# Kernel optimization log

Measured on AMD Instinct MI355X. Metric: run time of the kernel, lower is better.

Reference implementation:

```python
import jax, jax.numpy as jnp
import numpy as np

FORGET_BIAS = 1.0  # TF BasicLSTMCell default

B, T, D, H = 64, 1024, 300, 512


def setup_inputs() -> dict:
    key = jax.random.key(0)
    k1, k2, k3 = jax.random.split(key, 3)
    essays = jax.random.normal(k1, (B, T, D), dtype=jnp.float32)
    # TF BasicLSTMCell: single kernel [D+H, 4H], gate order (i, j, f, o)
    W_lstm = jax.random.normal(k2, (D + H, 4 * H), dtype=jnp.float32) * 0.05
    b_lstm = jnp.zeros((4 * H,), dtype=jnp.float32)
    W_dense = jax.random.normal(k3, (H, 1), dtype=jnp.float32) * 0.05
    b_dense = jnp.zeros((1,), dtype=jnp.float32)
    return {"essays": essays, "W_lstm": W_lstm, "b_lstm": b_lstm,
            "W_dense": W_dense, "b_dense": b_dense}


def _lstm_scan(essays, W_lstm, b_lstm):
    # Precompute input projection for all timesteps: [B,T,4H]
    Wx, Wh = W_lstm[:D], W_lstm[D:]
    x_proj = jnp.einsum('btd,dg->btg', essays, Wx) + b_lstm

    def step(carry, xp):
        c, h = carry
        gates = xp + h @ Wh  # [B,4H]
        i, j, f, o = jnp.split(gates, 4, axis=-1)
        new_c = c * jax.nn.sigmoid(f + FORGET_BIAS) + jax.nn.sigmoid(i) * jnp.tanh(j)
        new_h = jnp.tanh(new_c) * jax.nn.sigmoid(o)
        return (new_c, new_h), new_h

    init = (jnp.zeros((essays.shape[0], H), essays.dtype),
            jnp.zeros((essays.shape[0], H), essays.dtype))
    _, hs = jax.lax.scan(step, init, jnp.swapaxes(x_proj, 0, 1))  # hs: [T,B,H]
    return jnp.swapaxes(hs, 0, 1)  # [B,T,H]


def reference(essays, W_lstm, b_lstm, W_dense, b_dense):
    lstm_out = _lstm_scan(essays, W_lstm, b_lstm)      # [B,T,H]
    mot = jnp.mean(lstm_out, axis=1)                   # mean-over-time pooling [B,H]
    preds = jax.nn.sigmoid(mot @ W_dense + b_dense)    # [B,1]
    return preds.reshape(-1)                           # [B]
```

## Files before the change

kernel.cpp:

```cpp
#include <hip/hip_runtime.h>
#include <hip/hip_bf16.h>
#include <stdint.h>

#define B_   64
#define T_   1024
#define D_   300
#define H_   512
#define G4H  2048
#define KP   320

typedef __attribute__((ext_vector_type(8))) short short8;
typedef __attribute__((ext_vector_type(4))) float f32x4;
typedef unsigned long long ull;

__device__ __forceinline__ unsigned short f2bf(float v) {
    __hip_bfloat16 h = __float2bfloat16(v);
    return *reinterpret_cast<unsigned short*>(&h);
}
__device__ __forceinline__ float bf2f(unsigned u) {
    return __uint_as_float(u << 16);
}
__device__ __forceinline__ float sigm(float x) { return 1.f / (1.f + __expf(-x)); }
__device__ __forceinline__ float tanhfast(float x) {
    float e = __expf(2.f * x);
    return 1.f - 2.f / (e + 1.f);
}

#define ASYNC16(g, l)                                                        \
    __builtin_amdgcn_global_load_lds(                                        \
        (const __attribute__((address_space(1))) void*)(g),                  \
        (__attribute__((address_space(3))) void*)(l), 16, 0, 0)

__global__ void cvt_essays(const float* __restrict__ es, unsigned short* __restrict__ Ab) {
    unsigned i = blockIdx.x * 256u + threadIdx.x;
    unsigned row = i / KP;
    unsigned col = i - row * KP;
    float v = (col < D_) ? es[(size_t)row * D_ + col] : 0.f;
    Ab[i] = f2bf(v);
}

__global__ void cvt_misc(const float* __restrict__ Wl, unsigned short* __restrict__ Bt) {
    unsigned i = blockIdx.x * 256u + threadIdx.x;
    unsigned n = i / KP, k = i - n * KP;
    float v = (k < D_) ? Wl[(size_t)k * G4H + n] : 0.f;
    Bt[i] = f2bf(v);
}

__global__ void cvt_wh(const float* __restrict__ Wl, unsigned short* __restrict__ WhTg) {
    unsigned i = blockIdx.x * 256u + threadIdx.x;
    unsigned gc = i & 2047u, k = i >> 11;
    WhTg[(size_t)gc * 512 + k] = f2bf(Wl[(size_t)(300 + k) * G4H + gc]);
}

__global__ __launch_bounds__(256) void gemm_xp(
    const unsigned short* __restrict__ Ab,
    const unsigned short* __restrict__ Bt,
    const float* __restrict__ bias,
    unsigned short* __restrict__ xpr)
{
    __shared__ __align__(16) unsigned short Al[128 * 32];
    __shared__ __align__(16) unsigned short Bl[128 * 32];
    const int tid = threadIdx.x;
    const int w = tid >> 6, lane = tid & 63;
    const int ln = lane & 15, q = lane >> 4;
    const int bx = blockIdx.x;
    const int m0 = (bx >> 4) * 128;
    const int n0 = (bx & 15) * 128;
    const int wr = w >> 1, wc = w & 1;

    f32x4 acc[4][4];
#pragma unroll
    for (int i = 0; i < 4; i++)
#pragma unroll
        for (int j = 0; j < 4; j++) acc[i][j] = (f32x4){0.f, 0.f, 0.f, 0.f};

    for (int k0 = 0; k0 < KP; k0 += 32) {
#pragma unroll
        for (int it = 0; it < 2; ++it) {
            int s = it * 4 + w;
            int c = s * 64 + lane;
            int r = c >> 2;
            int ko = (c & 3) * 8;
            ASYNC16(Ab + (size_t)(m0 + r) * KP + k0 + ko, &Al[s * 512]);
            ASYNC16(Bt + (size_t)(n0 + r) * KP + k0 + ko, &Bl[s * 512]);
        }
        __syncthreads();
        short8 af[4], bf[4];
#pragma unroll
        for (int mt = 0; mt < 4; ++mt)
            af[mt] = *(const short8*)&Al[(wr * 64 + mt * 16 + ln) * 32 + q * 8];
#pragma unroll
        for (int nt = 0; nt < 4; ++nt)
            bf[nt] = *(const short8*)&Bl[(wc * 64 + nt * 16 + ln) * 32 + q * 8];
#pragma unroll
        for (int mt = 0; mt < 4; ++mt)
#pragma unroll
            for (int nt = 0; nt < 4; ++nt)
                acc[mt][nt] = __builtin_amdgcn_mfma_f32_16x16x32_bf16(af[mt], bf[nt], acc[mt][nt], 0, 0, 0);
        __syncthreads();
    }
#pragma unroll
    for (int mt = 0; mt < 4; ++mt) {
#pragma unroll
        for (int nt = 0; nt < 4; ++nt) {
            int col = n0 + wc * 64 + nt * 16 + ln;
            int gate = col >> 9, r9 = col & 511;
            int slice = r9 >> 4, jj = r9 & 15;
            float bb = bias[col];
#pragma unroll
            for (int r = 0; r < 4; ++r) {
                int row = m0 + wr * 64 + mt * 16 + q * 4 + r;
                int t = row & 1023, bglob = row >> 10;
                int g = bglob >> 4, bloc = bglob & 15;
                size_t idx = ((((size_t)t * 4 + g) * 32 + slice) * 16 + bloc) * 64
                             + gate * 16 + jj;
                xpr[idx] = f2bf(acc[mt][nt][r] + bb);
            }
        }
    }
}

__global__ __launch_bounds__(256, 1) void lstm_rec(
    const unsigned short* __restrict__ WhTg,
    const unsigned short* __restrict__ xpr,
    unsigned* __restrict__ hfp,
    float* __restrict__ hmean)
{
    __shared__ __align__(16) unsigned short WhT[64 * 520];
    __shared__ __align__(16) unsigned short hl[16 * 520];
    __shared__ float gbuf[4][16][17];

    const int tid = threadIdx.x;
    const int bid = blockIdx.x;
    const int g     = bid >> 5;
    const int slice = bid & 31;
    const int j0    = slice * 16;
    const int bg    = g * 16;
    const int wv = tid >> 6, lane = tid & 63, ln = lane & 15, q = lane >> 4;

    for (int ch = tid; ch < 64 * 64; ch += 256) {
        int c = ch >> 6, off = (ch & 63) * 8;
        int gc = (c >> 4) * 512 + j0 + (c & 15);
        *(uint4*)&WhT[c * 520 + off] = *(const uint4*)&WhTg[(size_t)gc * 512 + off];
    }

    const int b = tid >> 4;
    const int j = tid & 15;
    const int rowoff = (bg + b) * 512;

    {
        ull* hl8 = (ull*)hl;
#pragma unroll
        for (int i = 0; i < 16; ++i) {
            int c = tid + (i << 8);
            int row = c >> 8, pair = c & 255;
            hl8[(row * 1040 + pair * 8) >> 3] = 0ull;
        }
    }

    float c_st = 0.f, hsum = 0.f;
    const unsigned short* xblk0 = xpr + ((size_t)g * 32 + slice) * 1024 + b * 64 + j;
    unsigned short xc0 = xblk0[0], xc1 = xblk0[16], xc2 = xblk0[32], xc3 = xblk0[48];
    unsigned short xn0 = xc0, xn1 = xc1, xn2 = xc2, xn3 = xc3;

    for (int t = 0; t < T_; ++t) {
        if (t + 1 < T_) {
            const unsigned short* xr = xblk0 + (size_t)(t + 1) * 131072;
            xn0 = xr[0]; xn1 = xr[16]; xn2 = xr[32]; xn3 = xr[48];
        }
        if (t > 0) {
            const ull* src = (const ull*)(hfp + (size_t)(t & 1) * 32768 + bg * 512);
            const unsigned want = (unsigned)((t >> 1) & 3);
            ull v[16];
#pragma unroll
            for (int i = 0; i < 16; ++i)
                v[i] = __hip_atomic_load(src + tid + (i << 8),
                                         __ATOMIC_RELAXED, __HIP_MEMORY_SCOPE_AGENT);
            while (true) {
                unsigned bad = 0u;
#pragma unroll
                for (int i = 0; i < 16; ++i) {
                    unsigned lo = (unsigned)v[i], hi = (unsigned)(v[i] >> 32);
                    bad |= ((((lo & 3u) ^ want) | ((hi & 3u) ^ want)) != 0u) ? (1u << i) : 0u;
                }
                if (!bad) break;
#pragma unroll
                for (int i = 0; i < 16; ++i)
                    if (bad & (1u << i))
                        v[i] = __hip_atomic_load(src + tid + (i << 8),
                                                 __ATOMIC_RELAXED, __HIP_MEMORY_SCOPE_AGENT);
            }
#pragma unroll
            for (int i = 0; i < 16; ++i) {
                int c = tid + (i << 8);
                int row = c >> 8, pair = c & 255;
                unsigned u = (unsigned)f2bf(__uint_as_float((unsigned)v[i]))
                           | ((unsigned)f2bf(__uint_as_float((unsigned)(v[i] >> 32))) << 16);
                *(unsigned*)((char*)hl + row * 1040 + pair * 4) = u;
            }
        }
        __syncthreads();

        f32x4 acc = (f32x4){0.f, 0.f, 0.f, 0.f};
#pragma unroll
        for (int kk = 0; kk < 16; ++kk) {
            short8 av = *(const short8*)&hl[ln * 520 + kk * 32 + q * 8];
            short8 bv = *(const short8*)&WhT[(wv * 16 + ln) * 520 + kk * 32 + q * 8];
            acc = __builtin_amdgcn_mfma_f32_16x16x32_bf16(av, bv, acc, 0, 0, 0);
        }
#pragma unroll
        for (int r = 0; r < 4; ++r)
            gbuf[wv][q * 4 + r][ln] = acc[r];
        __syncthreads();

        float ai  = gbuf[0][b][j] + bf2f((unsigned)xc0);
        float aj  = gbuf[1][b][j] + bf2f((unsigned)xc1);
        float af_ = gbuf[2][b][j] + bf2f((unsigned)xc2);
        float ao  = gbuf[3][b][j] + bf2f((unsigned)xc3);
        float si = sigm(ai), tj = tanhfast(aj);
        float sf = sigm(af_ + 1.0f), so = sigm(ao);
        c_st = c_st * sf + si * tj;
        float h = tanhfast(c_st) * so;
        hsum += h;
        xc0 = xn0; xc1 = xn1; xc2 = xn2; xc3 = xn3;

        unsigned hb = (__float_as_uint(h) & ~3u) | (unsigned)(((t + 1) >> 1) & 3);
        __hip_atomic_store(hfp + (size_t)((t + 1) & 1) * 32768 + rowoff + j0 + j,
                           hb, __ATOMIC_RELAXED, __HIP_MEMORY_SCOPE_AGENT);
    }
    hmean[(size_t)rowoff + j0 + j] = hsum * (1.f / 1024.f);
}

__global__ void dense_out(const float* __restrict__ hmean, const float* __restrict__ Wd,
                          const float* __restrict__ bd, float* __restrict__ out) {
    int bb = blockIdx.x;
    int lane = threadIdx.x;
    float p = 0.f;
    for (int e = lane; e < H_; e += 64) p += hmean[(size_t)bb * H_ + e] * Wd[e];
#pragma unroll
    for (int off = 32; off; off >>= 1) p += __shfl_down(p, off);
    if (lane == 0) out[bb] = 1.f / (1.f + __expf(-(p + bd[0])));
}

extern "C" void kernel_launch(void* const* d_in, const int* in_sizes, int n_in,
                              void* d_out, int out_size, void* d_ws, size_t ws_size,
                              hipStream_t stream) {
    const float* essays  = (const float*)d_in[0];
    const float* W_lstm  = (const float*)d_in[1];
    const float* b_lstm  = (const float*)d_in[2];
    const float* W_dense = (const float*)d_in[3];
    const float* b_dense = (const float*)d_in[4];
    float* out = (float*)d_out;

    char* ws = (char*)d_ws;
    unsigned short* xp   = (unsigned short*)(ws);
    unsigned short* Ab   = (unsigned short*)(ws + 268435456ull);
    unsigned short* Bt   = (unsigned short*)(ws + 310378496ull);
    unsigned short* WhTg = (unsigned short*)(ws + 311689216ull);
    unsigned*       hfp  = (unsigned*)(ws + 268435456ull);
    float*          hm   = (float*)(ws + 268435456ull + 262144ull);

    hipLaunchKernelGGL(cvt_essays, dim3(81920), dim3(256), 0, stream, essays, Ab);
    hipLaunchKernelGGL(cvt_misc,   dim3(2560),  dim3(256), 0, stream, W_lstm, Bt);
    hipLaunchKernelGGL(cvt_wh,     dim3(4096),  dim3(256), 0, stream, W_lstm, WhTg);
    hipLaunchKernelGGL(gemm_xp,    dim3(8192),  dim3(256), 0, stream, Ab, Bt, b_lstm, xp);
    hipLaunchKernelGGL(lstm_rec,   dim3(128),   dim3(256), 0, stream, WhTg, xp, hfp, hm);
    hipLaunchKernelGGL(dense_out,  dim3(64),    dim3(64),  0, stream, hm, W_dense, b_dense, out);
}
```

Before: 3.620 ms.

## Restructure LSTM recurrence into single-wave blocks with register weights and swizzled bf16 h exchange

The recurrent kernel moves from 256-thread blocks to one 64-lane wave per block. The Wh slice now lives in registers instead of LDS, and all four gate accumulators are computed by the same wave, which removes both __syncthreads and the gate-staging buffer. Hidden state is exchanged as bf16 with a 16-bit timestep tag in a layout pre-swizzled to match the MFMA A-operand. Each chunk is polled and fed straight into the MFMA, so waiting overlaps with compute. The xproj layout is interleaved per gate for 64-bit loads. The trade-offs are heavy register pressure (64 short8 weights plus 64 ull loads) and a 16-bit tag that wraps only beyond 65535 steps.

```diff
diff --git a/kernel.cpp b/kernel.cpp
--- a/kernel.cpp
+++ b/kernel.cpp
@@ -31,6 +31,8 @@
         (const __attribute__((address_space(1))) void*)(g),                  \
         (__attribute__((address_space(3))) void*)(l), 16, 0, 0)
 
+#define ALD(p) __hip_atomic_load((p), __ATOMIC_RELAXED, __HIP_MEMORY_SCOPE_AGENT)
+
 __global__ void cvt_essays(const float* __restrict__ es, unsigned short* __restrict__ Ab) {
     unsigned i = blockIdx.x * 256u + threadIdx.x;
     unsigned row = i / KP;
@@ -46,10 +48,12 @@
     Bt[i] = f2bf(v);
 }
 
-__global__ void cvt_wh(const float* __restrict__ Wl, unsigned short* __restrict__ WhTg) {
+__global__ void cvt_wh(const float* __restrict__ Wl, unsigned short* __restrict__ WhTg,
+                       unsigned* __restrict__ hswz) {
     unsigned i = blockIdx.x * 256u + threadIdx.x;
     unsigned gc = i & 2047u, k = i >> 11;
     WhTg[(size_t)gc * 512 + k] = f2bf(Wl[(size_t)(300 + k) * G4H + gc]);
+    if (i < 65536u) hswz[i] = 0x0000FFFFu;
 }
 
 __global__ __launch_bounds__(256) void gemm_xp(
@@ -113,122 +117,122 @@
                 int t = row & 1023, bglob = row >> 10;
                 int g = bglob >> 4, bloc = bglob & 15;
                 size_t idx = ((((size_t)t * 4 + g) * 32 + slice) * 16 + bloc) * 64
-                             + gate * 16 + jj;
+                             + jj * 4 + gate;
                 xpr[idx] = f2bf(acc[mt][nt][r] + bb);
             }
         }
     }
 }
 
-__global__ __launch_bounds__(256, 1) void lstm_rec(
+__global__ __launch_bounds__(64, 1) void lstm_rec(
     const unsigned short* __restrict__ WhTg,
     const unsigned short* __restrict__ xpr,
-    unsigned* __restrict__ hfp,
+    unsigned* __restrict__ hswz,
     float* __restrict__ hmean)
 {
-    __shared__ __align__(16) unsigned short WhT[64 * 520];
-    __shared__ __align__(16) unsigned short hl[16 * 520];
-    __shared__ float gbuf[4][16][17];
-
-    const int tid = threadIdx.x;
     const int bid = blockIdx.x;
     const int g     = bid >> 5;
     const int slice = bid & 31;
     const int j0    = slice * 16;
     const int bg    = g * 16;
-    const int wv = tid >> 6, lane = tid & 63, ln = lane & 15, q = lane >> 4;
-
-    for (int ch = tid; ch < 64 * 64; ch += 256) {
-        int c = ch >> 6, off = (ch & 63) * 8;
-        int gc = (c >> 4) * 512 + j0 + (c & 15);
-        *(uint4*)&WhT[c * 520 + off] = *(const uint4*)&WhTg[(size_t)gc * 512 + off];
-    }
-
-    const int b = tid >> 4;
-    const int j = tid & 15;
-    const int rowoff = (bg + b) * 512;
-
-    {
-        ull* hl8 = (ull*)hl;
-#pragma unroll
-        for (int i = 0; i < 16; ++i) {
-            int c = tid + (i << 8);
-            int row = c >> 8, pair = c & 255;
-            hl8[(row * 1040 + pair * 8) >> 3] = 0ull;
-        }
-    }
-
-    float c_st = 0.f, hsum = 0.f;
-    const unsigned short* xblk0 = xpr + ((size_t)g * 32 + slice) * 1024 + b * 64 + j;
-    unsigned short xc0 = xblk0[0], xc1 = xblk0[16], xc2 = xblk0[32], xc3 = xblk0[48];
-    unsigned short xn0 = xc0, xn1 = xc1, xn2 = xc2, xn3 = xc3;
+    const int lane = threadIdx.x, ln = lane & 15, q = lane >> 4;
+
+    short8 bw[64];
+#pragma unroll
+    for (int gate = 0; gate < 4; ++gate)
+#pragma unroll
+        for (int kk = 0; kk < 16; ++kk)
+            bw[gate * 16 + kk] =
+                *(const short8*)&WhTg[(size_t)(gate * 512 + j0 + ln) * 512 + kk * 32 + q * 8];
+
+    float c_[4] = {0.f, 0.f, 0.f, 0.f};
+    float hs[4] = {0.f, 0.f, 0.f, 0.f};
+
+    const int csrc = g * 4096 + q * 64 + ln * 4;
+    const int kel = j0 + ln;
+    const int sdst = g * 8192 + (kel >> 5) * 512 + ((kel >> 3) & 3) * 128 + q * 32 + (kel & 7);
+
+    const unsigned short* xreg0 = xpr + ((size_t)g * 32 + slice) * 1024;
+    ull xc[4], xn[4];
+#pragma unroll
+    for (int r = 0; r < 4; ++r)
+        xc[r] = *(const ull*)(xreg0 + (4 * q + r) * 64 + ln * 4);
 
     for (int t = 0; t < T_; ++t) {
         if (t + 1 < T_) {
-            const unsigned short* xr = xblk0 + (size_t)(t + 1) * 131072;
-            xn0 = xr[0]; xn1 = xr[16]; xn2 = xr[32]; xn3 = xr[48];
-        }
+            const unsigned short* xr = xreg0 + (size_t)(t + 1) * 131072;
+#pragma unroll
+            for (int r = 0; r < 4; ++r)
+                xn[r] = *(const ull*)(xr + (4 * q + r) * 64 + ln * 4);
+        }
+
+        f32x4 acc0 = (f32x4){0.f, 0.f, 0.f, 0.f};
+        f32x4 acc1 = (f32x4){0.f, 0.f, 0.f, 0.f};
+        f32x4 acc2 = (f32x4){0.f, 0.f, 0.f, 0.f};
+        f32x4 acc3 = (f32x4){0.f, 0.f, 0.f, 0.f};
+
         if (t > 0) {
-            const ull* src = (const ull*)(hfp + (size_t)(t & 1) * 32768 + bg * 512);
-            const unsigned want = (unsigned)((t >> 1) & 3);
-            ull v[16];
-#pragma unroll
-            for (int i = 0; i < 16; ++i)
-                v[i] = __hip_atomic_load(src + tid + (i << 8),
-                                         __ATOMIC_RELAXED, __HIP_MEMORY_SCOPE_AGENT);
-            while (true) {
-                unsigned bad = 0u;
-#pragma unroll
-                for (int i = 0; i < 16; ++i) {
-                    unsigned lo = (unsigned)v[i], hi = (unsigned)(v[i] >> 32);
-                    bad |= ((((lo & 3u) ^ want) | ((hi & 3u) ^ want)) != 0u) ? (1u << i) : 0u;
+            const ull* hb = (const ull*)hswz + (size_t)(t & 1) * 16384 + csrc;
+            const unsigned wt = (unsigned)t;
+            ull v[64];
+#pragma unroll
+            for (int kk = 0; kk < 16; ++kk)
+#pragma unroll
+                for (int i = 0; i < 4; ++i)
+                    v[kk * 4 + i] = ALD(hb + kk * 256 + i);
+#pragma unroll
+            for (int kk = 0; kk < 16; ++kk) {
+                ull a0 = v[kk * 4], a1 = v[kk * 4 + 1], a2 = v[kk * 4 + 2], a3 = v[kk * 4 + 3];
+                unsigned bad =
+                    (((unsigned)a0 ^ wt) | ((unsigned)(a0 >> 32) ^ wt) |
+                     ((unsigned)a1 ^ wt) | ((unsigned)(a1 >> 32) ^ wt) |
+                     ((unsigned)a2 ^ wt) | ((unsigned)(a2 >> 32) ^ wt) |
+                     ((unsigned)a3 ^ wt) | ((unsigned)(a3 >> 32) ^ wt)) & 0xffffu;
+                while (bad != 0u) {
+                    a0 = ALD(hb + kk * 256);
+                    a1 = ALD(hb + kk * 256 + 1);
+                    a2 = ALD(hb + kk * 256 + 2);
+                    a3 = ALD(hb + kk * 256 + 3);
+                    bad =
+                        (((unsigned)a0 ^ wt) | ((unsigned)(a0 >> 32) ^ wt) |
+                         ((unsigned)a1 ^ wt) | ((unsigned)(a1 >> 32) ^ wt) |
+                         ((unsigned)a2 ^ wt) | ((unsigned)(a2 >> 32) ^ wt) |
+                         ((unsigned)a3 ^ wt) | ((unsigned)(a3 >> 32) ^ wt)) & 0xffffu;
                 }
-                if (!bad) break;
-#pragma unroll
-                for (int i = 0; i < 16; ++i)
-                    if (bad & (1u << i))
-                        v[i] = __hip_atomic_load(src + tid + (i << 8),
-                                                 __ATOMIC_RELAXED, __HIP_MEMORY_SCOPE_AGENT);
+                union { unsigned u[4]; short8 s; } cv;
+                cv.u[0] = __builtin_amdgcn_perm((unsigned)(a0 >> 32), (unsigned)a0, 0x07060302u);
+                cv.u[1] = __builtin_amdgcn_perm((unsigned)(a1 >> 32), (unsigned)a1, 0x07060302u);
+                cv.u[2] = __builtin_amdgcn_perm((unsigned)(a2 >> 32), (unsigned)a2, 0x07060302u);
+                cv.u[3] = __builtin_amdgcn_perm((unsigned)(a3 >> 32), (unsigned)a3, 0x07060302u);
+                short8 af = cv.s;
+                acc0 = __builtin_amdgcn_mfma_f32_16x16x32_bf16(af, bw[kk],      acc0, 0, 0, 0);
+                acc1 = __builtin_amdgcn_mfma_f32_16x16x32_bf16(af, bw[16 + kk], acc1, 0, 0, 0);
+                acc2 = __builtin_amdgcn_mfma_f32_16x16x32_bf16(af, bw[32 + kk], acc2, 0, 0, 0);
+                acc3 = __builtin_amdgcn_mfma_f32_16x16x32_bf16(af, bw[48 + kk], acc3, 0, 0, 0);
             }
-#pragma unroll
-            for (int i = 0; i < 16; ++i) {
-                int c = tid + (i << 8);
-                int row = c >> 8, pair = c & 255;
-                unsigned u = (unsigned)f2bf(__uint_as_float((unsigned)v[i]))
-                           | ((unsigned)f2bf(__uint_as_float((unsigned)(v[i] >> 32))) << 16);
-                *(unsigned*)((char*)hl + row * 1040 + pair * 4) = u;
-            }
-        }
-        __syncthreads();
-
-        f32x4 acc = (f32x4){0.f, 0.f, 0.f, 0.f};
-#pragma unroll
-        for (int kk = 0; kk < 16; ++kk) {
-            short8 av = *(const short8*)&hl[ln * 520 + kk * 32 + q * 8];
-            short8 bv = *(const short8*)&WhT[(wv * 16 + ln) * 520 + kk * 32 + q * 8];
-            acc = __builtin_amdgcn_mfma_f32_16x16x32_bf16(av, bv, acc, 0, 0, 0);
-        }
-#pragma unroll
-        for (int r = 0; r < 4; ++r)
-            gbuf[wv][q * 4 + r][ln] = acc[r];
-        __syncthreads();
-
-        float ai  = gbuf[0][b][j] + bf2f((unsigned)xc0);
-        float aj  = gbuf[1][b][j] + bf2f((unsigned)xc1);
-        float af_ = gbuf[2][b][j] + bf2f((unsigned)xc2);
-        float ao  = gbuf[3][b][j] + bf2f((unsigned)xc3);
-        float si = sigm(ai), tj = tanhfast(aj);
-        float sf = sigm(af_ + 1.0f), so = sigm(ao);
-        c_st = c_st * sf + si * tj;
-        float h = tanhfast(c_st) * so;
-        hsum += h;
-        xc0 = xn0; xc1 = xn1; xc2 = xn2; xc3 = xn3;
-
-        unsigned hb = (__float_as_uint(h) & ~3u) | (unsigned)(((t + 1) >> 1) & 3);
-        __hip_atomic_store(hfp + (size_t)((t + 1) & 1) * 32768 + rowoff + j0 + j,
-                           hb, __ATOMIC_RELAXED, __HIP_MEMORY_SCOPE_AGENT);
+        }
+
+        unsigned* hdst = hswz + (size_t)((t + 1) & 1) * 32768 + sdst;
+        const unsigned newtag = (unsigned)(t + 1);
+#pragma unroll
+        for (int r = 0; r < 4; ++r) {
+            float ai  = acc0[r] + bf2f((unsigned)xc[r] & 0xffffu);
+            float aj  = acc1[r] + bf2f(((unsigned)xc[r]) >> 16);
+            float af_ = acc2[r] + bf2f((unsigned)(xc[r] >> 32) & 0xffffu);
+            float ao  = acc3[r] + bf2f((unsigned)(xc[r] >> 48));
+            float si = sigm(ai), tj = tanhfast(aj);
+            float sf = sigm(af_ + 1.0f), so = sigm(ao);
+            c_[r] = c_[r] * sf + si * tj;
+            float h = tanhfast(c_[r]) * so;
+            hs[r] += h;
+            unsigned hv = ((unsigned)f2bf(h) << 16) | newtag;
+            __hip_atomic_store(hdst + r * 8, hv, __ATOMIC_RELAXED, __HIP_MEMORY_SCOPE_AGENT);
+            xc[r] = xn[r];
+        }
     }
-    hmean[(size_t)rowoff + j0 + j] = hsum * (1.f / 1024.f);
+#pragma unroll
+    for (int r = 0; r < 4; ++r)
+        hmean[(size_t)(bg + 4 * q + r) * 512 + j0 + ln] = hs[r] * (1.f / 1024.f);
 }
 
 __global__ void dense_out(const float* __restrict__ hmean, const float* __restrict__ Wd,
@@ -257,13 +261,13 @@
     unsigned short* Ab   = (unsigned short*)(ws + 268435456ull);
     unsigned short* Bt   = (unsigned short*)(ws + 310378496ull);
     unsigned short* WhTg = (unsigned short*)(ws + 311689216ull);
-    unsigned*       hfp  = (unsigned*)(ws + 268435456ull);
-    float*          hm   = (float*)(ws + 268435456ull + 262144ull);
+    unsigned*       hswz = (unsigned*)(ws + 313786368ull);
+    float*          hm   = (float*)(ws + 268435456ull);
 
     hipLaunchKernelGGL(cvt_essays, dim3(81920), dim3(256), 0, stream, essays, Ab);
     hipLaunchKernelGGL(cvt_misc,   dim3(2560),  dim3(256), 0, stream, W_lstm, Bt);
-    hipLaunchKernelGGL(cvt_wh,     dim3(4096),  dim3(256), 0, stream, W_lstm, WhTg);
+    hipLaunchKernelGGL(cvt_wh,     dim3(4096),  dim3(256), 0, stream, W_lstm, WhTg, hswz);
     hipLaunchKernelGGL(gemm_xp,    dim3(8192),  dim3(256), 0, stream, Ab, Bt, b_lstm, xp);
-    hipLaunchKernelGGL(lstm_rec,   dim3(128),   dim3(256), 0, stream, WhTg, xp, hfp, hm);
+    hipLaunchKernelGGL(lstm_rec,   dim3(128),   dim3(64),  0, stream, WhTg, xp, hswz, hm);
     hipLaunchKernelGGL(dense_out,  dim3(64),    dim3(64),  0, stream, hm, W_dense, b_dense, out);
 }
```

Measured after the change: 7.987 ms. 2.21x slower.
